# Performance work log

Measured on AMD Instinct MI355X. Metric: run time of the kernel, lower is better.

The kernel has to match this reference:

```python
import jax, jax.numpy as jnp
import numpy as np

B, V, N, E = 1, 4, 10000, 128000
HEADS, OUT_F = 4, 64
DIN = 64
D = HEADS * OUT_F  # 256
NEG_SLOPE = 0.2


def setup_inputs() -> dict:
    key = jax.random.key(0)
    ks = jax.random.split(key, 16)
    def w(k, shape, fan_in):
        return jax.random.normal(k, shape, dtype=jnp.float32) * (1.0 / np.sqrt(fan_in))
    x = jax.random.normal(ks[0], (B, V, N, DIN), dtype=jnp.float32)
    edge_index = jax.random.randint(ks[1], (2, E), 0, N, dtype=jnp.int32)
    inp = {"x": x, "edge_index": edge_index}
    # layer 1: DIN -> D
    inp["W1"] = w(ks[2], (DIN, D), DIN)
    inp["att1"] = w(ks[3], (HEADS, 2 * OUT_F), 2 * OUT_F)
    inp["qkv_w1"] = w(ks[4], (3 * D, D), D)
    inp["qkv_b1"] = jnp.zeros((3 * D,), jnp.float32)
    inp["out_w1"] = w(ks[5], (D, D), D)
    inp["out_b1"] = jnp.zeros((D,), jnp.float32)
    inp["bias1"] = jnp.zeros((D,), jnp.float32)
    # layer 2: D -> D
    inp["W2"] = w(ks[6], (D, D), D)
    inp["att2"] = w(ks[7], (HEADS, 2 * OUT_F), 2 * OUT_F)
    inp["qkv_w2"] = w(ks[8], (3 * D, D), D)
    inp["qkv_b2"] = jnp.zeros((3 * D,), jnp.float32)
    inp["out_w2"] = w(ks[9], (D, D), D)
    inp["out_b2"] = jnp.zeros((D,), jnp.float32)
    inp["bias2"] = jnp.zeros((D,), jnp.float32)
    return inp


def _mha(x, qkv_w, qkv_b, out_w, out_b, nh):
    # x: [S, L, Dm]; torch nn.MultiheadAttention with in_proj_weight [3Dm, Dm]
    S, L, Dm = x.shape
    hd = Dm // nh
    qkv = x @ qkv_w.T + qkv_b
    q, k, v = jnp.split(qkv, 3, axis=-1)
    q = q.reshape(S, L, nh, hd)
    k = k.reshape(S, L, nh, hd)
    v = v.reshape(S, L, nh, hd)
    logits = jnp.einsum('sqhd,skhd->shqk', q, k) / np.sqrt(hd).astype(np.float32)
    a = jax.nn.softmax(logits, axis=-1)
    o = jnp.einsum('shqk,skhd->sqhd', a, v).reshape(S, L, Dm)
    return o @ out_w.T + out_b


def _gat_layer(xf, src, dst, W, att, qkv_w, qkv_b, out_w, out_b, bias):
    # xf: [B*V, N, Din] -> returns [B, V, N, D]
    BV, Nn, _ = xf.shape
    h = (xf @ W).reshape(BV, Nn, HEADS, OUT_F)
    # leaky_relu(cat(h_src, h_dst)) is elementwise -> split att into src/dst halves
    hl = jnp.where(h > 0, h, NEG_SLOPE * h)
    s_src = jnp.einsum('bnhf,hf->bnh', hl, att[:, :OUT_F])
    s_dst = jnp.einsum('bnhf,hf->bnh', hl, att[:, OUT_F:])
    scores = (s_src[:, src] + s_dst[:, dst]).mean(axis=0)     # [Etot, H] (mean over B*V, as in source)
    wts = jax.nn.softmax(scores, axis=0)                       # GLOBAL softmax over all edges (as in source)
    weighted = (h[:, src] * wts[None, :, :, None]).reshape(BV, -1, HEADS * OUT_F)  # [BV, Etot, D]
    agg = jax.ops.segment_sum(jnp.moveaxis(weighted, 1, 0), dst, num_segments=Nn)  # [N, BV, D]
    hout = jnp.moveaxis(agg, 0, 1)                             # [BV, N, D] (concat=True)
    # inter-view mixing: MHA over the V axis per (batch, node)
    hm = hout.reshape(B, V, Nn, -1)
    ha = jnp.transpose(hm, (0, 2, 1, 3)).reshape(B * Nn, V, -1)
    hmix = _mha(ha, qkv_w, qkv_b, out_w, out_b, HEADS)
    hmix = jnp.transpose(hmix.reshape(B, Nn, V, -1), (0, 2, 1, 3))
    return hmix + bias


def reference(x, edge_index, W1, att1, qkv_w1, qkv_b1, out_w1, out_b1, bias1,
              W2, att2, qkv_w2, qkv_b2, out_w2, out_b2, bias2):
    sl = jnp.arange(N, dtype=edge_index.dtype)
    ei = jnp.concatenate([edge_index, jnp.stack([sl, sl])], axis=1)  # add self-loops
    src, dst = ei[0], ei[1]
    h = x.reshape(B * V, N, -1)
    h1 = _gat_layer(h, src, dst, W1, att1, qkv_w1, qkv_b1, out_w1, out_b1, bias1)
    h1 = jax.nn.elu(h1)
    h2 = _gat_layer(h1.reshape(B * V, N, -1), src, dst, W2, att2, qkv_w2, qkv_b2, out_w2, out_b2, bias2)
    return h2
```

## Files before the change

kernel.cpp:

```cpp
#include <hip/hip_runtime.h>

#define NN 10000
#define NPAD 10048
#define EE 128000
#define ETOT 138000
#define DD 256
#define DIN 64

typedef unsigned short u16;
typedef __attribute__((ext_vector_type(8))) short short8v;
typedef __attribute__((ext_vector_type(4))) float f32x4;

__device__ __forceinline__ u16 f2bf(float f) {
    union { float f; unsigned u; } a; a.f = f;
    unsigned r = a.u + 0x7fffu + ((a.u >> 16) & 1u);
    return (u16)(r >> 16);
}
__device__ __forceinline__ float bf2f(u16 b) {
    union { unsigned u; float f; } a; a.u = ((unsigned)b) << 16;
    return a.f;
}

__device__ __forceinline__ void gl2lds16(const void* g, void* l) {
    __builtin_amdgcn_global_load_lds((const __attribute__((address_space(1))) unsigned int*)g,
                                     (__attribute__((address_space(3))) unsigned int*)l, 16, 0, 0);
}


__global__ void split_k(const float* __restrict__ W, u16* __restrict__ H, u16* __restrict__ L, int total) {
    int i = blockIdx.x * 256 + threadIdx.x;
    if (i >= total) return;
    float f = W[i];
    u16 h = f2bf(f);
    H[i] = h;
    L[i] = f2bf(f - bf2f(h));
}

__global__ void transpose_split_k(const float* __restrict__ W, u16* __restrict__ H, u16* __restrict__ L,
                                  int R, int C) {
    int idx = blockIdx.x * 256 + threadIdx.x;
    if (idx >= R * C) return;
    int r = idx / C, c = idx % C;
    float f = W[idx];
    u16 h = f2bf(f);
    H[c * R + r] = h;
    L[c * R + r] = f2bf(f - bf2f(h));
}


__global__ void deg_k(const int* __restrict__ ei, int* __restrict__ deg, int E, int Etot) {
    int e = blockIdx.x * 256 + threadIdx.x;
    if (e >= Etot) return;
    int dn = (e < E) ? ei[E + e] : (e - E);
    atomicAdd(&deg[dn], 1);
}

__global__ __launch_bounds__(1024) void scan_k(const int* __restrict__ deg, int* __restrict__ offs,
                                               int* __restrict__ cursor, int Nn) {
    __shared__ int ps[1024];
    int t = threadIdx.x;
    int chunk = (Nn + 1023) >> 10;
    int i0 = t * chunk;
    int local = 0;
    for (int i = 0; i < chunk; i++) {
        int idx = i0 + i;
        if (idx < Nn) local += deg[idx];
    }
    ps[t] = local;
    __syncthreads();
    for (int off = 1; off < 1024; off <<= 1) {
        int v = 0;
        if (t >= off) v = ps[t - off];
        __syncthreads();
        if (t >= off) ps[t] += v;
        __syncthreads();
    }
    int run = ps[t] - local;
    for (int i = 0; i < chunk; i++) {
        int idx = i0 + i;
        if (idx < Nn) {
            offs[idx] = run;
            cursor[idx] = run;
            run += deg[idx];
        }
    }
}

__global__ void csr_fill_k(const int* __restrict__ ei, int* __restrict__ cursor,
                           int* __restrict__ csr_eid, int* __restrict__ csr_src, int E, int Etot) {
    int e = blockIdx.x * 256 + threadIdx.x;
    if (e >= Etot) return;
    int s, dn;
    if (e < E) { s = ei[e]; dn = ei[E + e]; }
    else { s = dn = e - E; }
    int pos = atomicAdd(&cursor[dn], 1);
    csr_eid[pos] = e;
    csr_src[pos] = s;
}


__global__ __launch_bounds__(256) void edge_scores_max_k(
    const int* __restrict__ ei, const float* __restrict__ asrc, const float* __restrict__ adst,
    float* __restrict__ sc, float* __restrict__ pmax, int E, int Etot) {
    int t = threadIdx.x;
    int total = Etot * 4;
    int gid = blockIdx.x * 256 + t;
    int stride = gridDim.x * 256;
    float m = -3.4e38f;
    for (int idx = gid; idx < total; idx += stride) {
        int e = idx >> 2, hd = idx & 3;
        int s, dn;
        if (e < E) { s = ei[e]; dn = ei[E + e]; }
        else { s = dn = e - E; }
        float v = asrc[s * 4 + hd] + adst[dn * 4 + hd];
        sc[idx] = v;
        m = fmaxf(m, v);
    }
    __shared__ float lds[256];
    lds[t] = m;
    __syncthreads();
    if (t < 4) {
        float r = -3.4e38f;
        for (int j = t; j < 256; j += 4) r = fmaxf(r, lds[j]);
        pmax[blockIdx.x * 4 + t] = r;
    }
}

__global__ void head_max2_k(const float* __restrict__ pmax, float* __restrict__ hmax, int nblocks) {
    int t = threadIdx.x;
    if (t < 4) {
        float r = -3.4e38f;
        for (int b = 0; b < nblocks; b++) r = fmaxf(r, pmax[b * 4 + t]);
        hmax[t] = r;
    }
}

__global__ __launch_bounds__(256) void exp_sum_k(float* __restrict__ sc, const float* __restrict__ hmax,
                                                 float* __restrict__ hsum, int total) {
    __shared__ float ls[4];
    int t = threadIdx.x;
    if (t < 4) ls[t] = 0.f;
    __syncthreads();
    int idx = blockIdx.x * 256 + t;
    if (idx < total) {
        int hd = idx & 3;
        float w = expf(sc[idx] - hmax[hd]);
        sc[idx] = w;
        atomicAdd(&ls[hd], w);
    }
    __syncthreads();
    if (t < 4) atomicAdd(&hsum[t], ls[t]);
}

__global__ void wsort_k(const int* __restrict__ csr_eid, const float* __restrict__ wts,
                        const float* __restrict__ hsum, float* __restrict__ ws, int Etot) {
    int idx = blockIdx.x * 256 + threadIdx.x;
    if (idx >= Etot * 4) return;
    int pos = idx >> 2, hd = idx & 3;
    ws[idx] = wts[csr_eid[pos] * 4 + hd] / hsum[hd];
}

__global__ __launch_bounds__(256) void agg2b_k(const u16* __restrict__ hB, const float* __restrict__ ws,
                                               const int* __restrict__ offs, const int* __restrict__ deg,
                                               const int* __restrict__ csr_src,
                                               u16* __restrict__ aggH, u16* __restrict__ aggL, int Nn) {
    int n = blockIdx.x, t = threadIdx.x, hd = t >> 6;
    int o0 = offs[n], dg = deg[n];
    float a0 = 0.f, a1 = 0.f, a2 = 0.f, a3 = 0.f;
    int p = 0;
    for (; p + 1 < dg; p += 2) {
        int s0 = csr_src[o0 + p], s1 = csr_src[o0 + p + 1];
        float w0 = ws[(o0 + p) * 4 + hd], w1 = ws[(o0 + p + 1) * 4 + hd];
        const u16* h0 = hB + (long)s0 * 1024 + t;
        const u16* h1 = hB + (long)s1 * 1024 + t;
        a0 += w0 * bf2f(h0[0]) + w1 * bf2f(h1[0]);
        a1 += w0 * bf2f(h0[256]) + w1 * bf2f(h1[256]);
        a2 += w0 * bf2f(h0[512]) + w1 * bf2f(h1[512]);
        a3 += w0 * bf2f(h0[768]) + w1 * bf2f(h1[768]);
    }
    if (p < dg) {
        int s0 = csr_src[o0 + p];
        float w0 = ws[(o0 + p) * 4 + hd];
        const u16* h0 = hB + (long)s0 * 1024 + t;
        a0 += w0 * bf2f(h0[0]);
        a1 += w0 * bf2f(h0[256]);
        a2 += w0 * bf2f(h0[512]);
        a3 += w0 * bf2f(h0[768]);
    }
    const long vp = (long)NPAD * DD;
    long ob = (long)n * DD + t;
    auto st = [&](float val, long idx) {
        u16 hb = f2bf(val);
        aggH[idx] = hb;
        aggL[idx] = f2bf(val - bf2f(hb));
    };
    st(a0, ob);
    st(a1, vp + ob);
    st(a2, 2 * vp + ob);
    st(a3, 3 * vp + ob);
}

template <int KK>
__global__ __launch_bounds__(256) void gemm_h(
    const u16* __restrict__ AH, const u16* __restrict__ AL,
    const u16* __restrict__ BH, const u16* __restrict__ BL,
    u16* __restrict__ CH, int M, int Nnodes,
    const float* __restrict__ attw, float* __restrict__ asrc, float* __restrict__ adst, int nwg) {
    __shared__ u16 S[2][4][4096];
    int orig = blockIdx.y * 2 + blockIdx.x;
    int qq = nwg >> 3, rr = nwg & 7;
    int xcd = orig & 7, pos = orig >> 3;
    int wg = (xcd < rr ? xcd * (qq + 1) : rr * (qq + 1) + (xcd - rr) * qq) + pos;
    int bx = wg & 1, by = wg >> 1;
    int row0 = by * 128, col0 = bx * 128;
    int t = threadIdx.x, lane = t & 63, wv = t >> 6;

    int d0 = (wv * 2) * 64 + lane, d1 = d0 + 64;
    int row_0 = d0 >> 2, gp_0 = d0 & 3;
    int row_1 = d1 >> 2, gp_1 = d1 & 3;
    int sw_0 = (gp_0 ^ ((row_0 >> 1) & 3)) << 3;
    int sw_1 = (gp_1 ^ ((row_1 >> 1) & 3)) << 3;
    long arow0 = (long)(row0 + row_0) * KK + sw_0;
    long arow1 = (long)(row0 + row_1) * KK + sw_1;
    long brow0 = (long)(col0 + row_0) * KK + sw_0;
    long brow1 = (long)(col0 + row_1) * KK + sw_1;
    int base0 = wv * 1024, base1 = base0 + 512;

    int wr = wv >> 1, wc = wv & 1, lm = lane & 15, lk = lane >> 4;
    const int gsw = (lk ^ ((lm >> 1) & 3)) * 8;

    f32x4 acc[4][4];
#pragma unroll
    for (int i = 0; i < 4; i++)
#pragma unroll
        for (int j = 0; j < 4; j++) acc[i][j] = (f32x4)(0.f);

#define STAGE_H(db, k0)                                \
    do {                                               \
        gl2lds16(AH + arow0 + (k0), &S[db][0][base0]); \
        gl2lds16(AL + arow0 + (k0), &S[db][1][base0]); \
        gl2lds16(BH + brow0 + (k0), &S[db][2][base0]); \
        gl2lds16(BL + brow0 + (k0), &S[db][3][base0]); \
        gl2lds16(AH + arow1 + (k0), &S[db][0][base1]); \
        gl2lds16(AL + arow1 + (k0), &S[db][1][base1]); \
        gl2lds16(BH + brow1 + (k0), &S[db][2][base1]); \
        gl2lds16(BL + brow1 + (k0), &S[db][3][base1]); \
    } while (0)

    STAGE_H(0, 0);
#pragma unroll
    for (int ks = 0; ks < KK / 32; ks++) {
        int cur = ks & 1;
        if (ks < KK / 32 - 1) {
            STAGE_H(cur ^ 1, (ks + 1) * 32);
            asm volatile("s_waitcnt vmcnt(8)" ::: "memory");
        } else {
            asm volatile("s_waitcnt vmcnt(0)" ::: "memory");
        }
        __builtin_amdgcn_s_barrier();
        asm volatile("" ::: "memory");
        const u16* AhS = S[cur][0];
        const u16* AlS = S[cur][1];
        const u16* BhS = S[cur][2];
        const u16* BlS = S[cur][3];
        short8v afh[4], afl[4], bfh[4], bfl[4];
#pragma unroll
        for (int i = 0; i < 4; i++) {
            int am_l = wr * 64 + i * 16 + lm;
            afh[i] = *(const short8v*)&AhS[am_l * 32 + gsw];
            afl[i] = *(const short8v*)&AlS[am_l * 32 + gsw];
            int bc_l = wc * 64 + i * 16 + lm;
            bfh[i] = *(const short8v*)&BhS[bc_l * 32 + gsw];
            bfl[i] = *(const short8v*)&BlS[bc_l * 32 + gsw];
        }
#pragma unroll
        for (int i = 0; i < 4; i++)
#pragma unroll
            for (int j = 0; j < 4; j++) {
                acc[i][j] = __builtin_amdgcn_mfma_f32_16x16x32_bf16(afh[i], bfh[j], acc[i][j], 0, 0, 0);
                acc[i][j] = __builtin_amdgcn_mfma_f32_16x16x32_bf16(afl[i], bfh[j], acc[i][j], 0, 0, 0);
                acc[i][j] = __builtin_amdgcn_mfma_f32_16x16x32_bf16(afh[i], bfl[j], acc[i][j], 0, 0, 0);
            }
        asm volatile("" ::: "memory");
        __builtin_amdgcn_s_barrier();
    }
#undef STAGE_H

#pragma unroll
    for (int i = 0; i < 4; i++) {
        int rowb = row0 + wr * 64 + i * 16 + lk * 4;
#pragma unroll
        for (int j = 0; j < 4; j++) {
            int col = col0 + wc * 64 + j * 16 + lm;
#pragma unroll
            for (int r = 0; r < 4; r++) {
                int mrow = rowb + r;
                if (mrow >= M) continue;
                int vv = mrow / Nnodes;
                int n = mrow - vv * Nnodes;
                CH[((long)n * 4 + vv) * 256 + col] = f2bf(acc[i][j][r]);
            }
        }
    }

    {
        int hd = (col0 >> 6) + wc;
        const float* attS = attw + hd * 128;
        const float* attD = attS + 64;
#pragma unroll
        for (int i = 0; i < 4; i++) {
            int rowb = row0 + wr * 64 + i * 16 + lk * 4;
#pragma unroll
            for (int r = 0; r < 4; r++) {
                int mrow = rowb + r;
                float sS = 0.f, sD = 0.f;
#pragma unroll
                for (int j = 0; j < 4; j++) {
                    float hv2 = acc[i][j][r];
                    float hl = hv2 > 0.f ? hv2 : 0.2f * hv2;
                    int f = j * 16 + lm;
                    sS += hl * attS[f];
                    sD += hl * attD[f];
                }
#pragma unroll
                for (int msk = 1; msk < 16; msk <<= 1) {
                    sS += __shfl_xor(sS, msk, 64);
                    sD += __shfl_xor(sD, msk, 64);
                }
                if (lm == 0 && mrow < M) {
                    int vv = mrow / Nnodes;
                    int n = mrow - vv * Nnodes;
                    atomicAdd(&asrc[n * 4 + hd], 0.25f * sS);
                    atomicAdd(&adst[n * 4 + hd], 0.25f * sD);
                }
            }
        }
    }
}

__global__ __launch_bounds__(256) void gemm_qk(
    const u16* __restrict__ AH, const u16* __restrict__ BH,
    const float* __restrict__ bias, u16* __restrict__ QK,
    int Mc, int nodeBase, int nwg) {
    __shared__ u16 S[2][2][4096];
    int orig = blockIdx.y * 4 + blockIdx.x;
    int qq = nwg >> 3, rr = nwg & 7;
    int xcd = orig & 7, pos = orig >> 3;
    int wg = (xcd < rr ? xcd * (qq + 1) : rr * (qq + 1) + (xcd - rr) * qq) + pos;
    int bx = wg & 3, by = wg >> 2;
    int row0 = by * 128, col0 = bx * 128;
    int t = threadIdx.x, lane = t & 63, wv = t >> 6;

    int d0 = (wv * 2) * 64 + lane, d1 = d0 + 64;
    int row_0 = d0 >> 2, gp_0 = d0 & 3;
    int row_1 = d1 >> 2, gp_1 = d1 & 3;
    int sw_0 = (gp_0 ^ ((row_0 >> 1) & 3)) << 3;
    int sw_1 = (gp_1 ^ ((row_1 >> 1) & 3)) << 3;
    int m_0 = row0 + row_0, m_1 = row0 + row_1;
    long arow0 = ((long)(m_0 & 3) * NPAD + nodeBase + (m_0 >> 2)) * 256 + sw_0;
    long arow1 = ((long)(m_1 & 3) * NPAD + nodeBase + (m_1 >> 2)) * 256 + sw_1;
    long brow0 = (long)(col0 + row_0) * 256 + sw_0;
    long brow1 = (long)(col0 + row_1) * 256 + sw_1;
    int base0 = wv * 1024, base1 = base0 + 512;

    int wr = wv >> 1, wc = wv & 1, lm = lane & 15, lk = lane >> 4;
    const int gsw = (lk ^ ((lm >> 1) & 3)) * 8;

    f32x4 acc[4][4];
#pragma unroll
    for (int i = 0; i < 4; i++)
#pragma unroll
        for (int j = 0; j < 4; j++) acc[i][j] = (f32x4)(0.f);

#define STAGE_QK(db, k0)                               \
    do {                                               \
        gl2lds16(AH + arow0 + (k0), &S[db][0][base0]); \
        gl2lds16(BH + brow0 + (k0), &S[db][1][base0]); \
        gl2lds16(AH + arow1 + (k0), &S[db][0][base1]); \
        gl2lds16(BH + brow1 + (k0), &S[db][1][base1]); \
    } while (0)

    STAGE_QK(0, 0);
    for (int ks = 0; ks < 8; ks++) {
        int cur = ks & 1;
        if (ks < 7) {
            STAGE_QK(cur ^ 1, (ks + 1) * 32);
            asm volatile("s_waitcnt vmcnt(4)" ::: "memory");
        } else {
            asm volatile("s_waitcnt vmcnt(0)" ::: "memory");
        }
        __builtin_amdgcn_s_barrier();
        asm volatile("" ::: "memory");
        const u16* AhS = S[cur][0];
        const u16* BhS = S[cur][1];
        short8v af[4], bf[4];
#pragma unroll
        for (int i = 0; i < 4; i++) {
            af[i] = *(const short8v*)&AhS[(wr * 64 + i * 16 + lm) * 32 + gsw];
            bf[i] = *(const short8v*)&BhS[(wc * 64 + i * 16 + lm) * 32 + gsw];
        }
#pragma unroll
        for (int i = 0; i < 4; i++)
#pragma unroll
            for (int j = 0; j < 4; j++)
                acc[i][j] = __builtin_amdgcn_mfma_f32_16x16x32_bf16(af[i], bf[j], acc[i][j], 0, 0, 0);
        asm volatile("" ::: "memory");
        __builtin_amdgcn_s_barrier();
    }
#undef STAGE_QK

#pragma unroll
    for (int i = 0; i < 4; i++) {
        int rowb = wr * 64 + i * 16 + lk * 4;
#pragma unroll
        for (int j = 0; j < 4; j++) {
            int col = col0 + wc * 64 + j * 16 + lm;
            float bb = bias[col];
#pragma unroll
            for (int r = 0; r < 4; r++) {
                int m = row0 + rowb + r;
                if (m >= Mc) continue;
                QK[(long)m * 512 + col] = f2bf(acc[i][j][r] + bb);
            }
        }
    }
}

__global__ __launch_bounds__(256) void gemm_vpv(
    const u16* __restrict__ AH, const u16* __restrict__ AL,
    const u16* __restrict__ BH, const u16* __restrict__ BL,
    const float* __restrict__ biasV, const float* __restrict__ aw,
    u16* __restrict__ PVH, u16* __restrict__ PVL,
    int Mc, int nodeBase, int nwg) {
    __shared__ u16 S[2][4][4096];
    __shared__ float awS[1024];
    int orig = blockIdx.y * 2 + blockIdx.x;
    int qq = nwg >> 3, rr = nwg & 7;
    int xcd = orig & 7, pos = orig >> 3;
    int wg = (xcd < rr ? xcd * (qq + 1) : rr * (qq + 1) + (xcd - rr) * qq) + pos;
    int bx = wg & 1, by = wg >> 1;
    int row0 = by * 128, col0 = bx * 128;
    int t = threadIdx.x, lane = t & 63, wv = t >> 6;

    int n0 = row0 >> 2, hd0 = col0 >> 6;
    for (int i = t; i < 1024; i += 256) {
        int ln2 = i >> 5, rest = i & 31, hdl = rest >> 4, q16 = rest & 15;
        awS[i] = aw[(long)(n0 + ln2) * 64 + (hd0 + hdl) * 16 + q16];
    }
    __syncthreads();

    int d0 = (wv * 2) * 64 + lane, d1 = d0 + 64;
    int row_0 = d0 >> 2, gp_0 = d0 & 3;
    int row_1 = d1 >> 2, gp_1 = d1 & 3;
    int sw_0 = (gp_0 ^ ((row_0 >> 1) & 3)) << 3;
    int sw_1 = (gp_1 ^ ((row_1 >> 1) & 3)) << 3;
    int m_0 = row0 + row_0, m_1 = row0 + row_1;
    long arow0 = ((long)(m_0 & 3) * NPAD + nodeBase + (m_0 >> 2)) * 256 + sw_0;
    long arow1 = ((long)(m_1 & 3) * NPAD + nodeBase + (m_1 >> 2)) * 256 + sw_1;
    long brow0 = (long)(col0 + row_0) * 256 + sw_0;
    long brow1 = (long)(col0 + row_1) * 256 + sw_1;
    int base0 = wv * 1024, base1 = base0 + 512;

    int wr = wv >> 1, wc = wv & 1, lm = lane & 15, lk = lane >> 4;
    const int gsw = (lk ^ ((lm >> 1) & 3)) * 8;

    f32x4 acc[4][4];
#pragma unroll
    for (int i = 0; i < 4; i++)
#pragma unroll
        for (int j = 0; j < 4; j++) acc[i][j] = (f32x4)(0.f);

#define STAGE_V(db, k0)                                \
    do {                                               \
        gl2lds16(AH + arow0 + (k0), &S[db][0][base0]); \
        gl2lds16(AL + arow0 + (k0), &S[db][1][base0]); \
        gl2lds16(BH + brow0 + (k0), &S[db][2][base0]); \
        gl2lds16(BL + brow0 + (k0), &S[db][3][base0]); \
        gl2lds16(AH + arow1 + (k0), &S[db][0][base1]); \
        gl2lds16(AL + arow1 + (k0), &S[db][1][base1]); \
        gl2lds16(BH + brow1 + (k0), &S[db][2][base1]); \
        gl2lds16(BL + brow1 + (k0), &S[db][3][base1]); \
    } while (0)

    STAGE_V(0, 0);
    for (int ks = 0; ks < 8; ks++) {
        int cur = ks & 1;
        if (ks < 7) {
            STAGE_V(cur ^ 1, (ks + 1) * 32);
            asm volatile("s_waitcnt vmcnt(8)" ::: "memory");
        } else {
            asm volatile("s_waitcnt vmcnt(0)" ::: "memory");
        }
        __builtin_amdgcn_s_barrier();
        asm volatile("" ::: "memory");
        const u16* AhS = S[cur][0];
        const u16* AlS = S[cur][1];
        const u16* BhS = S[cur][2];
        const u16* BlS = S[cur][3];
        short8v afh[4], afl[4], bfh[4], bfl[4];
#pragma unroll
        for (int i = 0; i < 4; i++) {
            int am_l = wr * 64 + i * 16 + lm;
            afh[i] = *(const short8v*)&AhS[am_l * 32 + gsw];
            afl[i] = *(const short8v*)&AlS[am_l * 32 + gsw];
            int bc_l = wc * 64 + i * 16 + lm;
            bfh[i] = *(const short8v*)&BhS[bc_l * 32 + gsw];
            bfl[i] = *(const short8v*)&BlS[bc_l * 32 + gsw];
        }
#pragma unroll
        for (int i = 0; i < 4; i++)
#pragma unroll
            for (int j = 0; j < 4; j++) {
                acc[i][j] = __builtin_amdgcn_mfma_f32_16x16x32_bf16(afh[i], bfh[j], acc[i][j], 0, 0, 0);
                acc[i][j] = __builtin_amdgcn_mfma_f32_16x16x32_bf16(afl[i], bfh[j], acc[i][j], 0, 0, 0);
                acc[i][j] = __builtin_amdgcn_mfma_f32_16x16x32_bf16(afh[i], bfl[j], acc[i][j], 0, 0, 0);
            }
        asm volatile("" ::: "memory");
        __builtin_amdgcn_s_barrier();
    }
#undef STAGE_V

#pragma unroll
    for (int i = 0; i < 4; i++) {
        int rowb = wr * 64 + i * 16 + lk * 4;
        int ln2 = (rowb >> 2);
        const float* ap = &awS[ln2 * 32 + wc * 16];
#pragma unroll
        for (int j = 0; j < 4; j++) {
            int c = col0 + wc * 64 + j * 16 + lm;
            float bb = biasV[c];
            float o0 = ap[0] * acc[i][j][0] + ap[1] * acc[i][j][1] + ap[2] * acc[i][j][2] + ap[3] * acc[i][j][3];
            float o1 = ap[4] * acc[i][j][0] + ap[5] * acc[i][j][1] + ap[6] * acc[i][j][2] + ap[7] * acc[i][j][3];
            float o2 = ap[8] * acc[i][j][0] + ap[9] * acc[i][j][1] + ap[10] * acc[i][j][2] + ap[11] * acc[i][j][3];
            float o3 = ap[12] * acc[i][j][0] + ap[13] * acc[i][j][1] + ap[14] * acc[i][j][2] + ap[15] * acc[i][j][3];
            float ov[4] = {o0 + bb, o1 + bb, o2 + bb, o3 + bb};
#pragma unroll
            for (int r = 0; r < 4; r++) {
                int m = row0 + rowb + r;
                if (m >= Mc) continue;
                u16 hb = f2bf(ov[r]);
                PVH[(long)m * 256 + c] = hb;
                PVL[(long)m * 256 + c] = f2bf(ov[r] - bf2f(hb));
            }
        }
    }
}

template <int ACT, int SPLITOUT>
__global__ __launch_bounds__(256) void gemm_out(
    const u16* __restrict__ AH, const u16* __restrict__ AL,
    const u16* __restrict__ BH, const u16* __restrict__ BL,
    const float* __restrict__ b1, const float* __restrict__ b2,
    float* __restrict__ C, u16* __restrict__ H1H, u16* __restrict__ H1L,
    int Mc, int Nnodes, int nodeBase, int nwg) {
    __shared__ u16 S[2][4][4096];
    int orig = blockIdx.y * 2 + blockIdx.x;
    int qq = nwg >> 3, rr = nwg & 7;
    int xcd = orig & 7, pos = orig >> 3;
    int wg = (xcd < rr ? xcd * (qq + 1) : rr * (qq + 1) + (xcd - rr) * qq) + pos;
    int bx = wg & 1, by = wg >> 1;
    int row0 = by * 128, col0 = bx * 128;
    int t = threadIdx.x, lane = t & 63, wv = t >> 6;

    int d0 = (wv * 2) * 64 + lane, d1 = d0 + 64;
    int row_0 = d0 >> 2, gp_0 = d0 & 3;
    int row_1 = d1 >> 2, gp_1 = d1 & 3;
    int sw_0 = (gp_0 ^ ((row_0 >> 1) & 3)) << 3;
    int sw_1 = (gp_1 ^ ((row_1 >> 1) & 3)) << 3;
    long arow0 = (long)(row0 + row_0) * 256 + sw_0;
    long arow1 = (long)(row0 + row_1) * 256 + sw_1;
    long brow0 = (long)(col0 + row_0) * 256 + sw_0;
    long brow1 = (long)(col0 + row_1) * 256 + sw_1;
    int base0 = wv * 1024, base1 = base0 + 512;

    int wr = wv >> 1, wc = wv & 1, lm = lane & 15, lk = lane >> 4;
    const int gsw = (lk ^ ((lm >> 1) & 3)) * 8;

    f32x4 acc[4][4];
#pragma unroll
    for (int i = 0; i < 4; i++)
#pragma unroll
        for (int j = 0; j < 4; j++) acc[i][j] = (f32x4)(0.f);

#define STAGE_O(db, k0)                                \
    do {                                               \
        gl2lds16(AH + arow0 + (k0), &S[db][0][base0]); \
        gl2lds16(AL + arow0 + (k0), &S[db][1][base0]); \
        gl2lds16(BH + brow0 + (k0), &S[db][2][base0]); \
        gl2lds16(BL + brow0 + (k0), &S[db][3][base0]); \
        gl2lds16(AH + arow1 + (k0), &S[db][0][base1]); \
        gl2lds16(AL + arow1 + (k0), &S[db][1][base1]); \
        gl2lds16(BH + brow1 + (k0), &S[db][2][base1]); \
        gl2lds16(BL + brow1 + (k0), &S[db][3][base1]); \
    } while (0)

    STAGE_O(0, 0);
    for (int ks = 0; ks < 8; ks++) {
        int cur = ks & 1;
        if (ks < 7) {
            STAGE_O(cur ^ 1, (ks + 1) * 32);
            asm volatile("s_waitcnt vmcnt(8)" ::: "memory");
        } else {
            asm volatile("s_waitcnt vmcnt(0)" ::: "memory");
        }
        __builtin_amdgcn_s_barrier();
        asm volatile("" ::: "memory");
        const u16* AhS = S[cur][0];
        const u16* AlS = S[cur][1];
        const u16* BhS = S[cur][2];
        const u16* BlS = S[cur][3];
        short8v afh[4], afl[4], bfh[4], bfl[4];
#pragma unroll
        for (int i = 0; i < 4; i++) {
            int am_l = wr * 64 + i * 16 + lm;
            afh[i] = *(const short8v*)&AhS[am_l * 32 + gsw];
            afl[i] = *(const short8v*)&AlS[am_l * 32 + gsw];
            int bc_l = wc * 64 + i * 16 + lm;
            bfh[i] = *(const short8v*)&BhS[bc_l * 32 + gsw];
            bfl[i] = *(const short8v*)&BlS[bc_l * 32 + gsw];
        }
#pragma unroll
        for (int i = 0; i < 4; i++)
#pragma unroll
            for (int j = 0; j < 4; j++) {
                acc[i][j] = __builtin_amdgcn_mfma_f32_16x16x32_bf16(afh[i], bfh[j], acc[i][j], 0, 0, 0);
                acc[i][j] = __builtin_amdgcn_mfma_f32_16x16x32_bf16(afl[i], bfh[j], acc[i][j], 0, 0, 0);
                acc[i][j] = __builtin_amdgcn_mfma_f32_16x16x32_bf16(afh[i], bfl[j], acc[i][j], 0, 0, 0);
            }
        asm volatile("" ::: "memory");
        __builtin_amdgcn_s_barrier();
    }
#undef STAGE_O

#pragma unroll
    for (int i = 0; i < 4; i++) {
        int rowb = wr * 64 + i * 16 + lk * 4;
#pragma unroll
        for (int j = 0; j < 4; j++) {
            int col = col0 + wc * 64 + j * 16 + lm;
            float bb = b1[col] + b2[col];
#pragma unroll
            for (int r = 0; r < 4; r++) {
                int m = row0 + rowb + r;
                if (m >= Mc) continue;
                long cphys = (long)(m & 3) * Nnodes + nodeBase + (m >> 2);
                float v = acc[i][j][r] + bb;
                if (ACT == 1) v = v > 0.f ? v : expm1f(v);
                if (SPLITOUT) {
                    u16 hb = f2bf(v);
                    H1H[cphys * 256 + col] = hb;
                    H1L[cphys * 256 + col] = f2bf(v - bf2f(hb));
                } else {
                    C[cphys * 256 + col] = v;
                }
            }
        }
    }
}

__global__ __launch_bounds__(256) void aw_k(const u16* __restrict__ QK, float* __restrict__ aw, int chunkN) {
    int t = threadIdx.x, lane = t & 63, w = t >> 6;
    int node = blockIdx.x * 4 + w;
    if (node >= chunkN) return;
    int vq = lane >> 4, hd = (lane >> 2) & 3, vk = lane & 3;
    const u16* qp = QK + (long)(node * 4 + vq) * 512 + hd * 64;
    const u16* kp = QK + (long)(node * 4 + vk) * 512 + 256 + hd * 64;
    float acc = 0.f;
#pragma unroll
    for (int d0 = 0; d0 < 64; d0 += 8) {
        short8v qv = *(const short8v*)(qp + d0);
        short8v kv = *(const short8v*)(kp + d0);
#pragma unroll
        for (int j = 0; j < 8; j++) acc += bf2f((u16)qv[j]) * bf2f((u16)kv[j]);
    }
    float l = acc * 0.125f;
    float m = l;
    m = fmaxf(m, __shfl_xor(m, 1, 64));
    m = fmaxf(m, __shfl_xor(m, 2, 64));
    float e = expf(l - m);
    float s = e;
    s += __shfl_xor(s, 1, 64);
    s += __shfl_xor(s, 2, 64);
    aw[(long)node * 64 + hd * 16 + vq * 4 + vk] = e / s;
}


extern "C" void kernel_launch(void* const* d_in, const int* in_sizes, int n_in,
                              void* d_out, int out_size, void* d_ws, size_t ws_size,
                              hipStream_t stream) {
    const float* x = (const float*)d_in[0];
    const int* ei = (const int*)d_in[1];
    const float* W1 = (const float*)d_in[2];
    const float* att1 = (const float*)d_in[3];
    const float* qkv_w1 = (const float*)d_in[4];
    const float* qkv_b1 = (const float*)d_in[5];
    const float* out_w1 = (const float*)d_in[6];
    const float* out_b1 = (const float*)d_in[7];
    const float* bias1 = (const float*)d_in[8];
    const float* W2 = (const float*)d_in[9];
    const float* att2 = (const float*)d_in[10];
    const float* qkv_w2 = (const float*)d_in[11];
    const float* qkv_b2 = (const float*)d_in[12];
    const float* out_w2 = (const float*)d_in[13];
    const float* out_b2 = (const float*)d_in[14];
    const float* bias2 = (const float*)d_in[15];
    float* out = (float*)d_out;

    const int Nn = NN, E = EE, Etot = ETOT;
    const int MROWS = 40064;

    char* wsB = (char*)d_ws;
    size_t off = 0;
    auto alloc = [&](size_t bytes) -> void* {
        void* p = wsB + off;
        off += (bytes + 255) & ~(size_t)255;
        return p;
    };
    u16* W1TH = (u16*)alloc((size_t)256 * 64 * 2);
    u16* W1TL = (u16*)alloc((size_t)256 * 64 * 2);
    u16* W2TH = (u16*)alloc((size_t)256 * 256 * 2);
    u16* W2TL = (u16*)alloc((size_t)256 * 256 * 2);
    u16* qw1H = (u16*)alloc((size_t)768 * 256 * 2);
    u16* qw1L = (u16*)alloc((size_t)768 * 256 * 2);
    u16* qw2H = (u16*)alloc((size_t)768 * 256 * 2);
    u16* qw2L = (u16*)alloc((size_t)768 * 256 * 2);
    u16* ow1H = (u16*)alloc((size_t)256 * 256 * 2);
    u16* ow1L = (u16*)alloc((size_t)256 * 256 * 2);
    u16* ow2H = (u16*)alloc((size_t)256 * 256 * 2);
    u16* ow2L = (u16*)alloc((size_t)256 * 256 * 2);
    u16* xH = (u16*)alloc((size_t)MROWS * 64 * 2);
    u16* xL = (u16*)alloc((size_t)MROWS * 64 * 2);
    u16* h1H = (u16*)alloc((size_t)MROWS * 256 * 2);
    u16* h1L = (u16*)alloc((size_t)MROWS * 256 * 2);
    u16* hbufB = (u16*)alloc((size_t)Nn * 4 * DD * 2);
    u16* aggH = (u16*)alloc((size_t)4 * NPAD * DD * 2);
    u16* aggL = (u16*)alloc((size_t)4 * NPAD * DD * 2);
    float* asrc = (float*)alloc((size_t)Nn * 4 * 4);
    float* adst = (float*)alloc((size_t)Nn * 4 * 4);
    float* wts = (float*)alloc((size_t)Etot * 4 * 4);
    float* wsorted = (float*)alloc((size_t)Etot * 4 * 4);
    float* hmax = (float*)alloc(4 * 4);
    float* hsum = (float*)alloc(4 * 4);
    float* pmax = (float*)alloc((size_t)256 * 4 * 4);
    int* deg = (int*)alloc((size_t)Nn * 4);
    int* offs = (int*)alloc((size_t)Nn * 4);
    int* cursor = (int*)alloc((size_t)Nn * 4);
    int* csr_eid = (int*)alloc((size_t)Etot * 4);
    int* csr_src = (int*)alloc((size_t)Etot * 4);

    auto aligned = [](size_t b) { return (b + 255) & ~(size_t)255; };
    auto mpad_of = [](int cN) { return ((cN * 4 + 127) / 128) * 128; };
    int nchunks = 40;
    {
        const int cands[8] = {1, 2, 4, 5, 8, 10, 20, 40};
        for (int ci = 0; ci < 8; ci++) {
            int cN = Nn / cands[ci];
            long mp = mpad_of(cN);
            size_t need = off + aligned((size_t)mp * 512 * 2) + 2 * aligned((size_t)mp * 256 * 2) +
                          aligned((size_t)(mp / 4) * 64 * 4);
            if (need <= ws_size) { nchunks = cands[ci]; break; }
        }
    }
    int chunkN = Nn / nchunks;
    int Mpad = mpad_of(chunkN);
    u16* QKb = (u16*)alloc((size_t)Mpad * 512 * 2);
    u16* PVH = (u16*)alloc((size_t)Mpad * 256 * 2);
    u16* PVL = (u16*)alloc((size_t)Mpad * 256 * 2);
    float* awb = (float*)alloc((size_t)(Mpad / 4) * 64 * 4);

    transpose_split_k<<<(64 * 256 + 255) / 256, 256, 0, stream>>>(W1, W1TH, W1TL, 64, 256);
    transpose_split_k<<<(256 * 256 + 255) / 256, 256, 0, stream>>>(W2, W2TH, W2TL, 256, 256);
    split_k<<<(768 * 256 + 255) / 256, 256, 0, stream>>>(qkv_w1, qw1H, qw1L, 768 * 256);
    split_k<<<(768 * 256 + 255) / 256, 256, 0, stream>>>(qkv_w2, qw2H, qw2L, 768 * 256);
    split_k<<<(256 * 256 + 255) / 256, 256, 0, stream>>>(out_w1, ow1H, ow1L, 256 * 256);
    split_k<<<(256 * 256 + 255) / 256, 256, 0, stream>>>(out_w2, ow2H, ow2L, 256 * 256);
    split_k<<<(40000 * 64 + 255) / 256, 256, 0, stream>>>(x, xH, xL, 40000 * 64);
    hipMemsetAsync(deg, 0, Nn * sizeof(int), stream);
    deg_k<<<(Etot + 255) / 256, 256, 0, stream>>>(ei, deg, E, Etot);
    scan_k<<<1, 1024, 0, stream>>>(deg, offs, cursor, Nn);
    csr_fill_k<<<(Etot + 255) / 256, 256, 0, stream>>>(ei, cursor, csr_eid, csr_src, E, Etot);

    auto scoresAndAgg = [&](const float* att) {
        edge_scores_max_k<<<256, 256, 0, stream>>>(ei, asrc, adst, wts, pmax, E, Etot);
        head_max2_k<<<1, 64, 0, stream>>>(pmax, hmax, 256);
        hipMemsetAsync(hsum, 0, 16, stream);
        exp_sum_k<<<(Etot * 4 + 255) / 256, 256, 0, stream>>>(wts, hmax, hsum, Etot * 4);
        wsort_k<<<(Etot * 4 + 255) / 256, 256, 0, stream>>>(csr_eid, wts, hsum, wsorted, Etot);
        agg2b_k<<<Nn, 256, 0, stream>>>(hbufB, wsorted, offs, deg, csr_src, aggH, aggL, Nn);
    };

    int gy = Mpad / 128;

    hipMemsetAsync(asrc, 0, (size_t)Nn * 4 * 4, stream);
    hipMemsetAsync(adst, 0, (size_t)Nn * 4 * 4, stream);
    gemm_h<64><<<dim3(2, 313), 256, 0, stream>>>(xH, xL, W1TH, W1TL, hbufB, 40000, Nn,
                                                 att1, asrc, adst, 626);
    scoresAndAgg(att1);
    for (int c = 0; c < nchunks; c++) {
        int nb = c * chunkN;
        int Mc = chunkN * 4;
        gemm_qk<<<dim3(4, gy), 256, 0, stream>>>(aggH, qw1H, qkv_b1, QKb, Mc, nb, 4 * gy);
        aw_k<<<(chunkN + 3) / 4, 256, 0, stream>>>(QKb, awb, chunkN);
        gemm_vpv<<<dim3(2, gy), 256, 0, stream>>>(aggH, aggL, qw1H + 512 * 256, qw1L + 512 * 256,
                                                  qkv_b1 + 512, awb, PVH, PVL, Mc, nb, 2 * gy);
        gemm_out<1, 1><<<dim3(2, gy), 256, 0, stream>>>(PVH, PVL, ow1H, ow1L, out_b1, bias1,
                                                        nullptr, h1H, h1L, Mc, Nn, nb, 2 * gy);
    }

    hipMemsetAsync(asrc, 0, (size_t)Nn * 4 * 4, stream);
    hipMemsetAsync(adst, 0, (size_t)Nn * 4 * 4, stream);
    gemm_h<256><<<dim3(2, 313), 256, 0, stream>>>(h1H, h1L, W2TH, W2TL, hbufB, 40000, Nn,
                                                  att2, asrc, adst, 626);
    scoresAndAgg(att2);
    for (int c = 0; c < nchunks; c++) {
        int nb = c * chunkN;
        int Mc = chunkN * 4;
        gemm_qk<<<dim3(4, gy), 256, 0, stream>>>(aggH, qw2H, qkv_b2, QKb, Mc, nb, 4 * gy);
        aw_k<<<(chunkN + 3) / 4, 256, 0, stream>>>(QKb, awb, chunkN);
        gemm_vpv<<<dim3(2, gy), 256, 0, stream>>>(aggH, aggL, qw2H + 512 * 256, qw2L + 512 * 256,
                                                  qkv_b2 + 512, awb, PVH, PVL, Mc, nb, 2 * gy);
        gemm_out<0, 0><<<dim3(2, gy), 256, 0, stream>>>(PVH, PVL, ow2H, ow2L, out_b2, bias2,
                                                        out, nullptr, nullptr, Mc, Nn, nb, 2 * gy);
    }
}
```

Baseline: 612.3 us.

## Drop split-bf16 compensation in node projection GEMMs and fold head-max into exp_sum

The node feature projection GEMM (gemm_h) now uses single bf16 operands instead of hi/lo split pairs. This halves LDS staging and cuts the MFMA count per tile from three to one. The x input and the layer-1 output h1 are stored only as bf16 high parts, so the low-part buffers and their writes go away. The separate head-max reduction kernel is merged into exp_sum_k, where each block recomputes the max from pmax, and the two asrc/adst memsets become one. The cost is lower numerical accuracy in the projection, and every exp_sum block redundantly reads 1024 partial maxima; the single memset also assumes adst sits directly after asrc in memory.

```diff
diff --git a/kernel.cpp b/kernel.cpp
--- a/kernel.cpp
+++ b/kernel.cpp
@@ -34,6 +34,12 @@
     u16 h = f2bf(f);
     H[i] = h;
     L[i] = f2bf(f - bf2f(h));
+}
+
+__global__ void cvt_k(const float* __restrict__ W, u16* __restrict__ H, int total) {
+    int i = blockIdx.x * 256 + threadIdx.x;
+    if (i >= total) return;
+    H[i] = f2bf(W[i]);
 }
 
 __global__ void transpose_split_k(const float* __restrict__ W, u16* __restrict__ H, u16* __restrict__ L,
@@ -126,25 +132,27 @@
     }
 }
 
-__global__ void head_max2_k(const float* __restrict__ pmax, float* __restrict__ hmax, int nblocks) {
+__global__ __launch_bounds__(256) void exp_sum_k(float* __restrict__ sc, const float* __restrict__ pmax,
+                                                 float* __restrict__ hsum, int total) {
+    __shared__ float red[256];
+    __shared__ float hm[4];
+    __shared__ float ls[4];
     int t = threadIdx.x;
+    float m = -3.4e38f;
+    for (int j = t; j < 1024; j += 256) m = fmaxf(m, pmax[j]);
+    red[t] = m;
+    if (t < 4) ls[t] = 0.f;
+    __syncthreads();
     if (t < 4) {
         float r = -3.4e38f;
-        for (int b = 0; b < nblocks; b++) r = fmaxf(r, pmax[b * 4 + t]);
-        hmax[t] = r;
-    }
-}
-
-__global__ __launch_bounds__(256) void exp_sum_k(float* __restrict__ sc, const float* __restrict__ hmax,
-                                                 float* __restrict__ hsum, int total) {
-    __shared__ float ls[4];
-    int t = threadIdx.x;
-    if (t < 4) ls[t] = 0.f;
+        for (int j = t; j < 256; j += 4) r = fmaxf(r, red[j]);
+        hm[t] = r;
+    }
     __syncthreads();
     int idx = blockIdx.x * 256 + t;
     if (idx < total) {
         int hd = idx & 3;
-        float w = expf(sc[idx] - hmax[hd]);
+        float w = expf(sc[idx] - hm[hd]);
         sc[idx] = w;
         atomicAdd(&ls[hd], w);
     }
@@ -202,11 +210,10 @@
 
 template <int KK>
 __global__ __launch_bounds__(256) void gemm_h(
-    const u16* __restrict__ AH, const u16* __restrict__ AL,
-    const u16* __restrict__ BH, const u16* __restrict__ BL,
+    const u16* __restrict__ AH, const u16* __restrict__ BH,
     u16* __restrict__ CH, int M, int Nnodes,
     const float* __restrict__ attw, float* __restrict__ asrc, float* __restrict__ adst, int nwg) {
-    __shared__ u16 S[2][4][4096];
+    __shared__ u16 S[2][2][4096];
     int orig = blockIdx.y * 2 + blockIdx.x;
     int qq = nwg >> 3, rr = nwg & 7;
     int xcd = orig & 7, pos = orig >> 3;
@@ -238,13 +245,9 @@
 #define STAGE_H(db, k0)                                \
     do {                                               \
         gl2lds16(AH + arow0 + (k0), &S[db][0][base0]); \
-        gl2lds16(AL + arow0 + (k0), &S[db][1][base0]); \
-        gl2lds16(BH + brow0 + (k0), &S[db][2][base0]); \
-        gl2lds16(BL + brow0 + (k0), &S[db][3][base0]); \
+        gl2lds16(BH + brow0 + (k0), &S[db][1][base0]); \
         gl2lds16(AH + arow1 + (k0), &S[db][0][base1]); \
-        gl2lds16(AL + arow1 + (k0), &S[db][1][base1]); \
-        gl2lds16(BH + brow1 + (k0), &S[db][2][base1]); \
-        gl2lds16(BL + brow1 + (k0), &S[db][3][base1]); \
+        gl2lds16(BH + brow1 + (k0), &S[db][1][base1]); \
     } while (0)
 
     STAGE_H(0, 0);
@@ -253,34 +256,25 @@
         int cur = ks & 1;
         if (ks < KK / 32 - 1) {
             STAGE_H(cur ^ 1, (ks + 1) * 32);
-            asm volatile("s_waitcnt vmcnt(8)" ::: "memory");
+            asm volatile("s_waitcnt vmcnt(4)" ::: "memory");
         } else {
             asm volatile("s_waitcnt vmcnt(0)" ::: "memory");
         }
         __builtin_amdgcn_s_barrier();
         asm volatile("" ::: "memory");
         const u16* AhS = S[cur][0];
-        const u16* AlS = S[cur][1];
-        const u16* BhS = S[cur][2];
-        const u16* BlS = S[cur][3];
-        short8v afh[4], afl[4], bfh[4], bfl[4];
+        const u16* BhS = S[cur][1];
+        short8v af[4], bf[4];
 #pragma unroll
         for (int i = 0; i < 4; i++) {
-            int am_l = wr * 64 + i * 16 + lm;
-            afh[i] = *(const short8v*)&AhS[am_l * 32 + gsw];
-            afl[i] = *(const short8v*)&AlS[am_l * 32 + gsw];
-            int bc_l = wc * 64 + i * 16 + lm;
-            bfh[i] = *(const short8v*)&BhS[bc_l * 32 + gsw];
-            bfl[i] = *(const short8v*)&BlS[bc_l * 32 + gsw];
+            af[i] = *(const short8v*)&AhS[(wr * 64 + i * 16 + lm) * 32 + gsw];
+            bf[i] = *(const short8v*)&BhS[(wc * 64 + i * 16 + lm) * 32 + gsw];
         }
 #pragma unroll
         for (int i = 0; i < 4; i++)
 #pragma unroll
-            for (int j = 0; j < 4; j++) {
-                acc[i][j] = __builtin_amdgcn_mfma_f32_16x16x32_bf16(afh[i], bfh[j], acc[i][j], 0, 0, 0);
-                acc[i][j] = __builtin_amdgcn_mfma_f32_16x16x32_bf16(afl[i], bfh[j], acc[i][j], 0, 0, 0);
-                acc[i][j] = __builtin_amdgcn_mfma_f32_16x16x32_bf16(afh[i], bfl[j], acc[i][j], 0, 0, 0);
-            }
+            for (int j = 0; j < 4; j++)
+                acc[i][j] = __builtin_amdgcn_mfma_f32_16x16x32_bf16(af[i], bf[j], acc[i][j], 0, 0, 0);
         asm volatile("" ::: "memory");
         __builtin_amdgcn_s_barrier();
     }
@@ -551,7 +545,7 @@
     const u16* __restrict__ AH, const u16* __restrict__ AL,
     const u16* __restrict__ BH, const u16* __restrict__ BL,
     const float* __restrict__ b1, const float* __restrict__ b2,
-    float* __restrict__ C, u16* __restrict__ H1H, u16* __restrict__ H1L,
+    float* __restrict__ C, u16* __restrict__ H1H,
     int Mc, int Nnodes, int nodeBase, int nwg) {
     __shared__ u16 S[2][4][4096];
     int orig = blockIdx.y * 2 + blockIdx.x;
@@ -647,9 +641,7 @@
                 float v = acc[i][j][r] + bb;
                 if (ACT == 1) v = v > 0.f ? v : expm1f(v);
                 if (SPLITOUT) {
-                    u16 hb = f2bf(v);
-                    H1H[cphys * 256 + col] = hb;
-                    H1L[cphys * 256 + col] = f2bf(v - bf2f(hb));
+                    H1H[cphys * 256 + col] = f2bf(v);
                 } else {
                     C[cphys * 256 + col] = v;
                 }
@@ -729,9 +721,7 @@
     u16* ow2H = (u16*)alloc((size_t)256 * 256 * 2);
     u16* ow2L = (u16*)alloc((size_t)256 * 256 * 2);
     u16* xH = (u16*)alloc((size_t)MROWS * 64 * 2);
-    u16* xL = (u16*)alloc((size_t)MROWS * 64 * 2);
     u16* h1H = (u16*)alloc((size_t)MROWS * 256 * 2);
-    u16* h1L = (u16*)alloc((size_t)MROWS * 256 * 2);
     u16* hbufB = (u16*)alloc((size_t)Nn * 4 * DD * 2);
     u16* aggH = (u16*)alloc((size_t)4 * NPAD * DD * 2);
     u16* aggL = (u16*)alloc((size_t)4 * NPAD * DD * 2);
@@ -739,7 +729,6 @@
     float* adst = (float*)alloc((size_t)Nn * 4 * 4);
     float* wts = (float*)alloc((size_t)Etot * 4 * 4);
     float* wsorted = (float*)alloc((size_t)Etot * 4 * 4);
-    float* hmax = (float*)alloc(4 * 4);
     float* hsum = (float*)alloc(4 * 4);
     float* pmax = (float*)alloc((size_t)256 * 4 * 4);
     int* deg = (int*)alloc((size_t)Nn * 4);
@@ -774,28 +763,25 @@
     split_k<<<(768 * 256 + 255) / 256, 256, 0, stream>>>(qkv_w2, qw2H, qw2L, 768 * 256);
     split_k<<<(256 * 256 + 255) / 256, 256, 0, stream>>>(out_w1, ow1H, ow1L, 256 * 256);
     split_k<<<(256 * 256 + 255) / 256, 256, 0, stream>>>(out_w2, ow2H, ow2L, 256 * 256);
-    split_k<<<(40000 * 64 + 255) / 256, 256, 0, stream>>>(x, xH, xL, 40000 * 64);
+    cvt_k<<<(40000 * 64 + 255) / 256, 256, 0, stream>>>(x, xH, 40000 * 64);
     hipMemsetAsync(deg, 0, Nn * sizeof(int), stream);
     deg_k<<<(Etot + 255) / 256, 256, 0, stream>>>(ei, deg, E, Etot);
     scan_k<<<1, 1024, 0, stream>>>(deg, offs, cursor, Nn);
     csr_fill_k<<<(Etot + 255) / 256, 256, 0, stream>>>(ei, cursor, csr_eid, csr_src, E, Etot);
 
-    auto scoresAndAgg = [&](const float* att) {
+    auto scoresAndAgg = [&]() {
         edge_scores_max_k<<<256, 256, 0, stream>>>(ei, asrc, adst, wts, pmax, E, Etot);
-        head_max2_k<<<1, 64, 0, stream>>>(pmax, hmax, 256);
         hipMemsetAsync(hsum, 0, 16, stream);
-        exp_sum_k<<<(Etot * 4 + 255) / 256, 256, 0, stream>>>(wts, hmax, hsum, Etot * 4);
+        exp_sum_k<<<(Etot * 4 + 255) / 256, 256, 0, stream>>>(wts, pmax, hsum, Etot * 4);
         wsort_k<<<(Etot * 4 + 255) / 256, 256, 0, stream>>>(csr_eid, wts, hsum, wsorted, Etot);
         agg2b_k<<<Nn, 256, 0, stream>>>(hbufB, wsorted, offs, deg, csr_src, aggH, aggL, Nn);
     };
 
     int gy = Mpad / 128;
 
-    hipMemsetAsync(asrc, 0, (size_t)Nn * 4 * 4, stream);
-    hipMemsetAsync(adst, 0, (size_t)Nn * 4 * 4, stream);
-    gemm_h<64><<<dim3(2, 313), 256, 0, stream>>>(xH, xL, W1TH, W1TL, hbufB, 40000, Nn,
-                                                 att1, asrc, adst, 626);
-    scoresAndAgg(att1);
+    hipMemsetAsync(asrc, 0, (size_t)Nn * 4 * 4 * 2, stream);
+    gemm_h<64><<<dim3(2, 313), 256, 0, stream>>>(xH, W1TH, hbufB, 40000, Nn, att1, asrc, adst, 626);
+    scoresAndAgg();
     for (int c = 0; c < nchunks; c++) {
         int nb = c * chunkN;
         int Mc = chunkN * 4;
@@ -804,14 +790,12 @@
         gemm_vpv<<<dim3(2, gy), 256, 0, stream>>>(aggH, aggL, qw1H + 512 * 256, qw1L + 512 * 256,
                                                   qkv_b1 + 512, awb, PVH, PVL, Mc, nb, 2 * gy);
         gemm_out<1, 1><<<dim3(2, gy), 256, 0, stream>>>(PVH, PVL, ow1H, ow1L, out_b1, bias1,
-                                                        nullptr, h1H, h1L, Mc, Nn, nb, 2 * gy);
-    }
-
-    hipMemsetAsync(asrc, 0, (size_t)Nn * 4 * 4, stream);
-    hipMemsetAsync(adst, 0, (size_t)Nn * 4 * 4, stream);
-    gemm_h<256><<<dim3(2, 313), 256, 0, stream>>>(h1H, h1L, W2TH, W2TL, hbufB, 40000, Nn,
-                                                  att2, asrc, adst, 626);
-    scoresAndAgg(att2);
+                                                        nullptr, h1H, Mc, Nn, nb, 2 * gy);
+    }
+
+    hipMemsetAsync(asrc, 0, (size_t)Nn * 4 * 4 * 2, stream);
+    gemm_h<256><<<dim3(2, 313), 256, 0, stream>>>(h1H, W2TH, hbufB, 40000, Nn, att2, asrc, adst, 626);
+    scoresAndAgg();
     for (int c = 0; c < nchunks; c++) {
         int nb = c * chunkN;
         int Mc = chunkN * 4;
@@ -820,6 +804,6 @@
         gemm_vpv<<<dim3(2, gy), 256, 0, stream>>>(aggH, aggL, qw2H + 512 * 256, qw2L + 512 * 256,
                                                   qkv_b2 + 512, awb, PVH, PVL, Mc, nb, 2 * gy);
         gemm_out<0, 0><<<dim3(2, gy), 256, 0, stream>>>(PVH, PVL, ow2H, ow2L, out_b2, bias2,
-                                                        out, nullptr, nullptr, Mc, Nn, nb, 2 * gy);
-    }
-}
+                                                        out, nullptr, Mc, Nn, nb, 2 * gy);
+    }
+}
```

After: 558.9 us. 1.1x faster.
